# Kernel optimization log

Hardware: AMD Instinct MI355X
Metric: run time of the kernel (lower is better)

Reference implementation:

```python
import jax, jax.numpy as jnp
import numpy as np

H, W = 576, 640            # image_height, image_width
V = 5                      # visible_patch_width (z-buffer visibility window)
P = 7                      # color_path_width (color splat window)
EPS = 1e-5                 # epsilon in splat weight denominator
BIG = 1e10                 # empty-pixel depth sentinel


def setup_inputs():
    key = jax.random.key(0)
    ks = jax.random.split(key, 6)
    B, N = 1, 200000
    x = jax.random.uniform(ks[0], (B, N), jnp.float32) * W
    y = jax.random.uniform(ks[1], (B, N), jnp.float32) * H
    z = jax.random.uniform(ks[2], (B, N), jnp.float32) * 9.0 + 1.0
    proj_points = jnp.stack([x, y, z], axis=-1)                 # [B,N,3]
    proj_color = jax.random.uniform(ks[3], (B, N, 3), jnp.float32)
    Imweights = jax.random.uniform(ks[4], (B, N, 1), jnp.float32)
    mask = jax.random.randint(ks[5], (B, N), 0, 2).astype(jnp.int32)
    threshold = jnp.array([0.05], dtype=jnp.float32)
    return {"proj_points": proj_points, "proj_color": proj_color,
            "Imweights": Imweights, "mask": mask, "threshold": threshold}


def _render(proj_points, proj_color, Imweights, mask, th):
    B, N, _ = proj_points.shape
    dt = proj_points.dtype
    x, y, z = proj_points[..., 0], proj_points[..., 1], proj_points[..., 2]
    px = jnp.floor(x).astype(jnp.int32)          # [B,N]
    py = jnp.floor(y).astype(jnp.int32)
    valid = (px >= 0) & (px < W) & (py >= 0) & (py < H) & (mask > 0)

    # ---- z-buffer: per-pixel min depth (scatter-min) ----
    flat = jnp.clip(py, 0, H - 1) * W + jnp.clip(px, 0, W - 1)   # [B,N]
    bidx = jnp.arange(B)[:, None]
    zput = jnp.where(valid, z, BIG)
    depth = jnp.full((B, H * W), BIG, dt).at[bidx, flat].min(zput).reshape(B, H, W)

    # min depth within VxV visibility patch around each pixel
    patch_min = jax.lax.reduce_window(depth, jnp.asarray(BIG, dt), jax.lax.min,
                                      (1, V, V), (1, 1, 1), "SAME")
    pm = patch_min[bidx, jnp.clip(py, 0, H - 1), jnp.clip(px, 0, W - 1)]  # [B,N]
    is_visible = jax.lax.stop_gradient(valid & (z <= pm + th))

    # ---- PxP color splat with inverse-square-distance weights ----
    r = P // 2
    offs = jnp.arange(-r, r + 1)
    oy, ox = [o.ravel() for o in jnp.meshgrid(offs, offs, indexing="ij")]  # [K]
    sx = px[..., None] + ox                                     # [B,N,K]
    sy = py[..., None] + oy
    inb = (sx >= 0) & (sx < W) & (sy >= 0) & (sy < H) & is_visible[..., None]
    dx = sx.astype(dt) + 0.5 - x[..., None]
    dy = sy.astype(dt) + 0.5 - y[..., None]
    w = jnp.where(inb, 1.0 / (dx * dx + dy * dy + EPS), 0.0)    # [B,N,K]
    sflat = jnp.clip(sy, 0, H - 1) * W + jnp.clip(sx, 0, W - 1)
    b3 = jnp.arange(B)[:, None, None]

    weight_image = jnp.zeros((B, H * W), dt).at[b3, sflat].add(w).reshape(B, H, W)
    color_image = (jnp.zeros((B, H * W, proj_color.shape[-1]), dt)
                   .at[b3, sflat].add(w[..., None] * proj_color[:, :, None, :])
                   .reshape(B, H, W, proj_color.shape[-1]))
    Imweights_image = (jnp.zeros((B, H * W, Imweights.shape[-1]), dt)
                       .at[b3, sflat].add(w[..., None] * Imweights[:, :, None, :])
                       .reshape(B, H, W, Imweights.shape[-1]))
    depth_image = jnp.where(depth >= BIG, jnp.zeros((), dt), depth)
    return depth_image, color_image, Imweights_image, weight_image, is_visible


def reference(proj_points, proj_color, Imweights, mask, threshold):
    th = jnp.reshape(threshold, ())
    return _render(proj_points, proj_color, Imweights, mask, th)
```

## Files before the change

kernel.cpp:

```cpp
#include <hip/hip_runtime.h>
#include <math.h>

#define IMG_H 576
#define IMG_W 640
#define IMG_HW (IMG_H * IMG_W)
#define BIGF 1e10f
#define EPSF 1e-5f

#define TS 16
#define TX (IMG_W / TS)
#define TY (IMG_H / TS)
#define NT (TX * TY)
#define CAP 512

#define PBX 32
#define PBY 8
#define LW (PBX + 4)
#define LH (PBY + 4)


__global__ void init_kernel(unsigned int* depth_bits, unsigned int* counters) {
    int i = blockIdx.x * blockDim.x + threadIdx.x;
    if (i < IMG_HW) depth_bits[i] = __float_as_uint(BIGF);
    if (i < NT) counters[i] = 0u;
}

__global__ void zbuf_kernel(const float* __restrict__ pts, const int* __restrict__ mask,
                            unsigned int* depth_bits, int N) {
    int n = blockIdx.x * blockDim.x + threadIdx.x;
    if (n >= N) return;
    float x = pts[3 * n + 0];
    float y = pts[3 * n + 1];
    float z = pts[3 * n + 2];
    int px = (int)floorf(x);
    int py = (int)floorf(y);
    if (px >= 0 && px < IMG_W && py >= 0 && py < IMG_H && mask[n] > 0)
        atomicMin(&depth_bits[py * IMG_W + px], __float_as_uint(z));
}

__global__ void __launch_bounds__(256)
patchmin_kernel(const unsigned int* __restrict__ depth_bits,
                float* __restrict__ patch_min) {
    __shared__ float lds[LH * LW];
    int bx = (blockIdx.x % (IMG_W / PBX)) * PBX;
    int by = (blockIdx.x / (IMG_W / PBX)) * PBY;
    int tid = threadIdx.x;
    for (int i = tid; i < LH * LW; i += 256) {
        int gx = bx - 2 + (i % LW);
        int gy = by - 2 + (i / LW);
        float v = BIGF;
        if (gx >= 0 && gx < IMG_W && gy >= 0 && gy < IMG_H)
            v = __uint_as_float(depth_bits[gy * IMG_W + gx]);
        lds[i] = v;
    }
    __syncthreads();
    int lx = tid & (PBX - 1);
    int ly = tid >> 5;
    float m = BIGF;
    #pragma unroll
    for (int dy = 0; dy < 5; ++dy) {
        const float* row = lds + (ly + dy) * LW + lx;
        #pragma unroll
        for (int dx = 0; dx < 5; ++dx) m = fminf(m, row[dx]);
    }
    patch_min[(by + ly) * IMG_W + bx + lx] = m;
}

__global__ void vis_fill_kernel(const float* __restrict__ pts, const int* __restrict__ mask,
                                const float* __restrict__ thr,
                                const float* __restrict__ patch_min,
                                unsigned int* __restrict__ counters,
                                unsigned int* __restrict__ entries,
                                float* __restrict__ out_vis, int N) {
    int n = blockIdx.x * blockDim.x + threadIdx.x;
    if (n >= N) return;
    float x = pts[3 * n + 0];
    float y = pts[3 * n + 1];
    float z = pts[3 * n + 2];
    int px = (int)floorf(x);
    int py = (int)floorf(y);
    bool valid = (px >= 0) && (px < IMG_W) && (py >= 0) && (py < IMG_H) && (mask[n] > 0);
    bool vis = false;
    if (valid) {
        float pm = patch_min[py * IMG_W + px];
        vis = (z <= pm + thr[0]);
    }
    out_vis[n] = vis ? 1.0f : 0.0f;
    if (!vis) return;
    int xs0 = max(px - 3, 0), xs1 = min(px + 3, IMG_W - 1);
    int ys0 = max(py - 3, 0), ys1 = min(py + 3, IMG_H - 1);
    int tx0 = xs0 >> 4, tx1 = xs1 >> 4;
    int ty0 = ys0 >> 4, ty1 = ys1 >> 4;
    for (int ty = ty0; ty <= ty1; ++ty)
        for (int tx = tx0; tx <= tx1; ++tx) {
            int t = ty * TX + tx;
            unsigned int idx = atomicAdd(&counters[t], 1u);
            if (idx < CAP) entries[t * CAP + idx] = (unsigned int)n;
        }
}

__global__ void __launch_bounds__(256)
tile_splat_kernel(const float* __restrict__ pts, const float* __restrict__ color,
                  const float* __restrict__ imw,
                  const unsigned int* __restrict__ counters,
                  const unsigned int* __restrict__ entries,
                  const unsigned int* __restrict__ depth_bits,
                  float* __restrict__ out) {
    __shared__ float sx_[256], sy_[256], sr_[256], sg_[256], sb_[256], si_[256];
    int tile = blockIdx.x;
    int tx0p = (tile % TX) * TS;
    int ty0p = (tile / TX) * TS;
    int tid = threadIdx.x;
    int lx = tid & (TS - 1);
    int ly = tid >> 4;
    int gx = tx0p + lx;
    int gy = ty0p + ly;
    float pxf = (float)gx + 0.5f;
    float pyf = (float)gy + 0.5f;

    float aW = 0.0f, aI = 0.0f, aR = 0.0f, aG = 0.0f, aB = 0.0f;

    unsigned int count = min(counters[tile], (unsigned int)CAP);
    const unsigned int* list = entries + tile * CAP;

    for (unsigned int base = 0; base < count; base += 256u) {
        unsigned int chunk = min(256u, count - base);
        __syncthreads();
        if (tid < chunk) {
            int n = (int)list[base + tid];
            sx_[tid] = pts[3 * n + 0];
            sy_[tid] = pts[3 * n + 1];
            sr_[tid] = color[3 * n + 0];
            sg_[tid] = color[3 * n + 1];
            sb_[tid] = color[3 * n + 2];
            si_[tid] = imw[n];
        }
        __syncthreads();
        for (unsigned int e = 0; e < chunk; ++e) {
            float x = sx_[e];
            float y = sy_[e];
            int px = (int)floorf(x);
            int py = (int)floorf(y);
            if ((unsigned int)(gx - px + 3) <= 6u && (unsigned int)(gy - py + 3) <= 6u) {
                float dx = pxf - x;
                float dy = pyf - y;
                float w = 1.0f / (dx * dx + dy * dy + EPSF);
                aW += w;
                aI += w * si_[e];
                aR += w * sr_[e];
                aG += w * sg_[e];
                aB += w * sb_[e];
            }
        }
    }

    int p = gy * IMG_W + gx;
    float d0 = __uint_as_float(depth_bits[p]);
    out[p] = (d0 >= BIGF) ? 0.0f : d0;
    float* colimg = out + IMG_HW;
    colimg[3 * p + 0] = aR;
    colimg[3 * p + 1] = aG;
    colimg[3 * p + 2] = aB;
    out[4 * IMG_HW + p] = aI;
    out[5 * IMG_HW + p] = aW;
}

extern "C" void kernel_launch(void* const* d_in, const int* in_sizes, int n_in,
                              void* d_out, int out_size, void* d_ws, size_t ws_size,
                              hipStream_t stream) {
    const float* pts   = (const float*)d_in[0];
    const float* color = (const float*)d_in[1];
    const float* imw   = (const float*)d_in[2];
    const int*   mask  = (const int*)d_in[3];
    const float* thr   = (const float*)d_in[4];

    int N = in_sizes[3];

    unsigned int* ws_u = (unsigned int*)d_ws;
    unsigned int* depth_bits = ws_u;
    float*        patch_min  = (float*)(ws_u + IMG_HW);
    unsigned int* counters   = ws_u + 2 * IMG_HW;
    unsigned int* entries    = counters + NT;

    float* out = (float*)d_out;
    float* out_vis = out + 6 * IMG_HW;

    const int B = 256;
    init_kernel<<<(IMG_HW + B - 1) / B, B, 0, stream>>>(depth_bits, counters);
    zbuf_kernel<<<(N + B - 1) / B, B, 0, stream>>>(pts, mask, depth_bits, N);
    patchmin_kernel<<<(IMG_W / PBX) * (IMG_H / PBY), 256, 0, stream>>>(depth_bits, patch_min);
    vis_fill_kernel<<<(N + B - 1) / B, B, 0, stream>>>(pts, mask, thr, patch_min,
                                                       counters, entries, out_vis, N);
    tile_splat_kernel<<<NT, 256, 0, stream>>>(pts, color, imw, counters, entries,
                                              depth_bits, out);
}
```

Measured before the change: 94.04 us.

## Fold patch-min into visibility kernel and drop the init and patch-min kernels

Removes the separate patch-min pass: each valid point now gathers the 5x5 depth neighbourhood straight from the z-buffer in the visibility kernel. The init kernel is replaced by a byte memset that uses the all-ones uint as the empty sentinel, and the counter reset moves into the z-buffer kernel. The splat kernel also stores the precomputed floor of each point's coordinates in shared memory, so the inner loop no longer recomputes it. This saves two kernel launches and a full-image intermediate buffer. In exchange it issues about 25 scattered loads per valid point instead of one pass over the image.

```diff
diff --git a/kernel.cpp b/kernel.cpp
--- a/kernel.cpp
+++ b/kernel.cpp
@@ -13,21 +13,13 @@
 #define NT (TX * TY)
 #define CAP 512
 
-#define PBX 32
-#define PBY 8
-#define LW (PBX + 4)
-#define LH (PBY + 4)
 
-
-__global__ void init_kernel(unsigned int* depth_bits, unsigned int* counters) {
-    int i = blockIdx.x * blockDim.x + threadIdx.x;
-    if (i < IMG_HW) depth_bits[i] = __float_as_uint(BIGF);
-    if (i < NT) counters[i] = 0u;
-}
-
-__global__ void zbuf_kernel(const float* __restrict__ pts, const int* __restrict__ mask,
-                            unsigned int* depth_bits, int N) {
+__global__ void __launch_bounds__(256)
+zbuf_kernel(const float* __restrict__ pts, const int* __restrict__ mask,
+            unsigned int* __restrict__ depth_bits,
+            unsigned int* __restrict__ counters, int N) {
     int n = blockIdx.x * blockDim.x + threadIdx.x;
+    if (n < NT) counters[n] = 0u;
     if (n >= N) return;
     float x = pts[3 * n + 0];
     float y = pts[3 * n + 1];
@@ -39,39 +31,12 @@
 }
 
 __global__ void __launch_bounds__(256)
-patchmin_kernel(const unsigned int* __restrict__ depth_bits,
-                float* __restrict__ patch_min) {
-    __shared__ float lds[LH * LW];
-    int bx = (blockIdx.x % (IMG_W / PBX)) * PBX;
-    int by = (blockIdx.x / (IMG_W / PBX)) * PBY;
-    int tid = threadIdx.x;
-    for (int i = tid; i < LH * LW; i += 256) {
-        int gx = bx - 2 + (i % LW);
-        int gy = by - 2 + (i / LW);
-        float v = BIGF;
-        if (gx >= 0 && gx < IMG_W && gy >= 0 && gy < IMG_H)
-            v = __uint_as_float(depth_bits[gy * IMG_W + gx]);
-        lds[i] = v;
-    }
-    __syncthreads();
-    int lx = tid & (PBX - 1);
-    int ly = tid >> 5;
-    float m = BIGF;
-    #pragma unroll
-    for (int dy = 0; dy < 5; ++dy) {
-        const float* row = lds + (ly + dy) * LW + lx;
-        #pragma unroll
-        for (int dx = 0; dx < 5; ++dx) m = fminf(m, row[dx]);
-    }
-    patch_min[(by + ly) * IMG_W + bx + lx] = m;
-}
-
-__global__ void vis_fill_kernel(const float* __restrict__ pts, const int* __restrict__ mask,
-                                const float* __restrict__ thr,
-                                const float* __restrict__ patch_min,
-                                unsigned int* __restrict__ counters,
-                                unsigned int* __restrict__ entries,
-                                float* __restrict__ out_vis, int N) {
+vis_fill_kernel(const float* __restrict__ pts, const int* __restrict__ mask,
+                const float* __restrict__ thr,
+                const unsigned int* __restrict__ depth_bits,
+                unsigned int* __restrict__ counters,
+                unsigned int* __restrict__ entries,
+                float* __restrict__ out_vis, int N) {
     int n = blockIdx.x * blockDim.x + threadIdx.x;
     if (n >= N) return;
     float x = pts[3 * n + 0];
@@ -82,8 +47,20 @@
     bool valid = (px >= 0) && (px < IMG_W) && (py >= 0) && (py < IMG_H) && (mask[n] > 0);
     bool vis = false;
     if (valid) {
-        float pm = patch_min[py * IMG_W + px];
-        vis = (z <= pm + thr[0]);
+        int xs[5], ys[5];
+        #pragma unroll
+        for (int k = 0; k < 5; ++k) {
+            xs[k] = min(max(px + k - 2, 0), IMG_W - 1);
+            ys[k] = min(max(py + k - 2, 0), IMG_H - 1) * IMG_W;
+        }
+        unsigned int pm = 0xFFFFFFFFu;
+        #pragma unroll
+        for (int dy = 0; dy < 5; ++dy) {
+            const unsigned int* row = depth_bits + ys[dy];
+            #pragma unroll
+            for (int dx = 0; dx < 5; ++dx) pm = min(pm, row[xs[dx]]);
+        }
+        vis = (z <= __uint_as_float(pm) + thr[0]);
     }
     out_vis[n] = vis ? 1.0f : 0.0f;
     if (!vis) return;
@@ -107,6 +84,7 @@
                   const unsigned int* __restrict__ depth_bits,
                   float* __restrict__ out) {
     __shared__ float sx_[256], sy_[256], sr_[256], sg_[256], sb_[256], si_[256];
+    __shared__ int spx_[256], spy_[256];
     int tile = blockIdx.x;
     int tx0p = (tile % TX) * TS;
     int ty0p = (tile / TX) * TS;
@@ -126,10 +104,14 @@
     for (unsigned int base = 0; base < count; base += 256u) {
         unsigned int chunk = min(256u, count - base);
         __syncthreads();
-        if (tid < chunk) {
+        if (tid < (int)chunk) {
             int n = (int)list[base + tid];
-            sx_[tid] = pts[3 * n + 0];
-            sy_[tid] = pts[3 * n + 1];
+            float x = pts[3 * n + 0];
+            float y = pts[3 * n + 1];
+            sx_[tid] = x;
+            sy_[tid] = y;
+            spx_[tid] = (int)floorf(x);
+            spy_[tid] = (int)floorf(y);
             sr_[tid] = color[3 * n + 0];
             sg_[tid] = color[3 * n + 1];
             sb_[tid] = color[3 * n + 2];
@@ -137,13 +119,11 @@
         }
         __syncthreads();
         for (unsigned int e = 0; e < chunk; ++e) {
-            float x = sx_[e];
-            float y = sy_[e];
-            int px = (int)floorf(x);
-            int py = (int)floorf(y);
+            int px = spx_[e];
+            int py = spy_[e];
             if ((unsigned int)(gx - px + 3) <= 6u && (unsigned int)(gy - py + 3) <= 6u) {
-                float dx = pxf - x;
-                float dy = pyf - y;
+                float dx = pxf - sx_[e];
+                float dy = pyf - sy_[e];
                 float w = 1.0f / (dx * dx + dy * dy + EPSF);
                 aW += w;
                 aI += w * si_[e];
@@ -155,8 +135,8 @@
     }
 
     int p = gy * IMG_W + gx;
-    float d0 = __uint_as_float(depth_bits[p]);
-    out[p] = (d0 >= BIGF) ? 0.0f : d0;
+    unsigned int d_bits = depth_bits[p];
+    out[p] = (d_bits >= __float_as_uint(BIGF)) ? 0.0f : __uint_as_float(d_bits);
     float* colimg = out + IMG_HW;
     colimg[3 * p + 0] = aR;
     colimg[3 * p + 1] = aG;
@@ -178,18 +158,16 @@
 
     unsigned int* ws_u = (unsigned int*)d_ws;
     unsigned int* depth_bits = ws_u;
-    float*        patch_min  = (float*)(ws_u + IMG_HW);
-    unsigned int* counters   = ws_u + 2 * IMG_HW;
+    unsigned int* counters   = ws_u + IMG_HW;
     unsigned int* entries    = counters + NT;
 
     float* out = (float*)d_out;
     float* out_vis = out + 6 * IMG_HW;
 
     const int B = 256;
-    init_kernel<<<(IMG_HW + B - 1) / B, B, 0, stream>>>(depth_bits, counters);
-    zbuf_kernel<<<(N + B - 1) / B, B, 0, stream>>>(pts, mask, depth_bits, N);
-    patchmin_kernel<<<(IMG_W / PBX) * (IMG_H / PBY), 256, 0, stream>>>(depth_bits, patch_min);
-    vis_fill_kernel<<<(N + B - 1) / B, B, 0, stream>>>(pts, mask, thr, patch_min,
+    hipMemsetAsync(depth_bits, 0xFF, (size_t)IMG_HW * 4, stream);
+    zbuf_kernel<<<(N + B - 1) / B, B, 0, stream>>>(pts, mask, depth_bits, counters, N);
+    vis_fill_kernel<<<(N + B - 1) / B, B, 0, stream>>>(pts, mask, thr, depth_bits,
                                                        counters, entries, out_vis, N);
     tile_splat_kernel<<<NT, 256, 0, stream>>>(pts, color, imw, counters, entries,
                                               depth_bits, out);
```

Measured after the change: 93.89 us. About the same (-0.2%).
